# Optimization experiments

Hardware: AMD Instinct MI355X
Metric: run time of the kernel (lower is better)

## Reference

```python
import jax, jax.numpy as jnp
import numpy as np

N, E = 50000, 800000
IN_DIM, HID, HEADS, NUM_CLASSES, NUM_GRAPHS, NUM_LAYERS = 64, 64, 4, 10000, 256, 3
OUT_W = HID * HEADS  # 256


def _gat_layer(x, src, dst, W, a_src, a_dst, b, n_nodes):
    # x: [N, in], W: [heads*out, in], a_src/a_dst: [heads, out], b: [heads*out]
    h = (x @ W.T).reshape(n_nodes, HEADS, HID)            # [N, H, D]
    s_src = jnp.einsum('nhd,hd->nh', h, a_src)            # [N, H]
    s_dst = jnp.einsum('nhd,hd->nh', h, a_dst)
    alpha = jax.nn.leaky_relu(s_src[src] + s_dst[dst], 0.2)  # [E, H]
    m = jax.ops.segment_max(alpha, dst, num_segments=n_nodes)
    m = jnp.where(jnp.isfinite(m), m, 0.0)                # isolated-node safety
    ex = jnp.exp(alpha - m[dst])
    denom = jax.ops.segment_sum(ex, dst, num_segments=n_nodes)
    w = ex / (denom[dst] + 1e-16)                         # PyG softmax epsilon
    out = jax.ops.segment_sum(h[src] * w[:, :, None], dst, num_segments=n_nodes)
    return out.reshape(n_nodes, HEADS * HID) + b


def setup_inputs() -> dict:
    key = jax.random.key(0)
    ks = jax.random.split(key, 20)
    inp = {
        'x': jax.random.normal(ks[0], (N, IN_DIM), jnp.float32),
        'edge_index': jax.random.randint(ks[1], (2, E), 0, N, jnp.int32),
        'batch': jnp.sort(jax.random.randint(ks[2], (N,), 0, NUM_GRAPHS, jnp.int32)),
        'class_label': jax.random.randint(ks[3], (NUM_GRAPHS,), 0, NUM_CLASSES, jnp.int32),
        'emb': jax.random.normal(ks[4], (NUM_CLASSES, HID), jnp.float32),
    }
    in_dims = [IN_DIM + HID, OUT_W, OUT_W]
    for l in range(NUM_LAYERS):
        kw = jax.random.split(ks[5 + l], 4)
        d_in = in_dims[l]
        sc = 1.0 / np.sqrt(d_in)
        inp[f'W{l}'] = jax.random.uniform(kw[0], (OUT_W, d_in), jnp.float32, -sc, sc)
        inp[f'asrc{l}'] = jax.random.uniform(kw[1], (HEADS, HID), jnp.float32, -sc, sc)
        inp[f'adst{l}'] = jax.random.uniform(kw[2], (HEADS, HID), jnp.float32, -sc, sc)
        inp[f'b{l}'] = jnp.zeros((OUT_W,), jnp.float32)
    sc = 1.0 / np.sqrt(OUT_W)
    inp['cls_W'] = jax.random.uniform(ks[10], (1, OUT_W), jnp.float32, -sc, sc)
    inp['cls_b'] = jnp.zeros((1,), jnp.float32)
    return inp


def reference(x, edge_index, batch, class_label, emb,
              W0, asrc0, adst0, b0,
              W1, asrc1, adst1, b1,
              W2, asrc2, adst2, b2,
              cls_W, cls_b):
    n = x.shape[0]
    # template embedding aligned per node
    t = emb[class_label][batch]                          # [N, HID]
    h = jnp.concatenate([x, t], axis=-1)                 # [N, IN+HID]
    # PyG GATConv adds self-loops by default
    loop = jnp.arange(n, dtype=edge_index.dtype)
    src = jnp.concatenate([edge_index[0], loop])
    dst = jnp.concatenate([edge_index[1], loop])
    params = [(W0, asrc0, adst0, b0), (W1, asrc1, adst1, b1), (W2, asrc2, adst2, b2)]
    for (W, a_s, a_d, b) in params:
        h = _gat_layer(h, src, dst, W, a_s, a_d, b, n)
        h = jax.nn.leaky_relu(h, 0.01)                   # F.leaky_relu default slope
    return h @ cls_W.T + cls_b                           # [N, 1]
```

## Files before the change

### kernel.cpp

```cpp
#include <hip/hip_runtime.h>
#include <hip/hip_bf16.h>
#include <hip/hip_fp16.h>
#include <math.h>

#define NNODES 50000
#define NEDGES 800000
#define NBLK 196

typedef __attribute__((ext_vector_type(8))) _Float16 f16x8;
typedef __attribute__((ext_vector_type(4))) _Float16 f16x4;
typedef __attribute__((ext_vector_type(4))) float f32x4;

static __device__ __forceinline__ void gl_lds16(const void* g, void* l) {
    __builtin_amdgcn_global_load_lds(
        (const __attribute__((address_space(1))) void*)g,
        (__attribute__((address_space(3))) void*)l, 16, 0, 0);
}

__global__ void zero_int_kernel(int* __restrict__ p, int n) {
    int i = blockIdx.x * blockDim.x + threadIdx.x;
    if (i < n) p[i] = 0;
}

__global__ void bucket_kernel(const int* __restrict__ ei,
                              int* __restrict__ deg,
                              int* __restrict__ slots) {
    int e = blockIdx.x * blockDim.x + threadIdx.x;
    if (e >= NEDGES) return;
    int d = ei[NEDGES + e];
    int p = atomicAdd(&deg[d], 1);
    if (p < 64) slots[(size_t)d * 64 + p] = ei[e];
}

__global__ void prep_kernel(const float* __restrict__ x,
                            const int* __restrict__ batch,
                            const int* __restrict__ class_label,
                            const float* __restrict__ emb,
                            const float* __restrict__ W0,
                            const float* __restrict__ W1,
                            const float* __restrict__ W2,
                            _Float16* __restrict__ h0,
                            _Float16* __restrict__ F0,
                            _Float16* __restrict__ F1,
                            _Float16* __restrict__ F2) {
    int idx = blockIdx.x * blockDim.x + threadIdx.x;
    const int NH0 = NNODES * 128;
    if (idx < NH0) {
        int n = idx >> 7, c = idx & 127;
        float v;
        if (c < 64) v = x[(n << 6) + c];
        else        v = emb[class_label[batch[n]] * 64 + (c - 64)];
        h0[idx] = (_Float16)v;
    } else {
        int i = idx - NH0;
        if (i < 32768)        F0[i] = (_Float16)W0[i];
        else if (i < 98304)   F1[i - 32768] = (_Float16)W1[i - 32768];
        else if (i < 163840)  F2[i - 98304] = (_Float16)W2[i - 98304];
    }
}

template <int K>
__global__ __launch_bounds__(256) void gemm_mfma_kernel(
        const _Float16* __restrict__ A, const _Float16* __restrict__ W,
        const float* __restrict__ a_src, const float* __restrict__ a_dst,
        _Float16* __restrict__ Cf,
        float* __restrict__ ssrc, float* __restrict__ sdst) {
    __shared__ _Float16 sA[128 * 64];
    __shared__ _Float16 sB[128 * 64];
    const int M = NNODES;
    int tid = threadIdx.x;
    int lane = tid & 63, wave = tid >> 6;
    int wm = wave >> 1, wn = wave & 1;
    int l16 = lane & 15, quad = lane >> 4;
    int bm = blockIdx.x * 128, bn = blockIdx.y * 128;

    int rsub = lane >> 3;
    int kcs = (lane & 7) ^ rsub;
    int sw = l16 & 7;

    f32x4 acc[4][4];
#pragma unroll
    for (int r = 0; r < 4; ++r)
#pragma unroll
        for (int c = 0; c < 4; ++c) acc[r][c] = (f32x4){0.f, 0.f, 0.f, 0.f};

    const int NST = K / 64;
#pragma unroll
    for (int s = 0; s < NST; ++s) {
        int ks = s * 64;
        __syncthreads();
#pragma unroll
        for (int j = 0; j < 4; ++j) {
            int seg = wave * 4 + j;
            int r = seg * 8 + rsub;
            int acol = ks + kcs * 8;
            int garow = bm + r; if (garow > M - 1) garow = M - 1;
            gl_lds16(A + (size_t)garow * K + acol, &sA[seg * 512]);
            gl_lds16(W + (size_t)(bn + r) * K + acol, &sB[seg * 512]);
        }
        __syncthreads();
#pragma unroll
        for (int ks32 = 0; ks32 < 2; ++ks32) {
            f16x8 af[4], bf[4];
#pragma unroll
            for (int r = 0; r < 4; ++r) {
                int row = wm * 64 + r * 16 + l16;
                af[r] = *(const f16x8*)&sA[row * 64 + ((ks32 * 4 + quad) ^ sw) * 8];
            }
#pragma unroll
            for (int c = 0; c < 4; ++c) {
                int row = wn * 64 + c * 16 + l16;
                bf[c] = *(const f16x8*)&sB[row * 64 + ((ks32 * 4 + quad) ^ sw) * 8];
            }
#pragma unroll
            for (int r = 0; r < 4; ++r)
#pragma unroll
                for (int c = 0; c < 4; ++c)
                    acc[r][c] = __builtin_amdgcn_mfma_f32_16x16x32_f16(
                        af[r], bf[c], acc[r][c], 0, 0, 0);
        }
    }

    int headblk = (bn + wn * 64) >> 6;
    float asv[4], adv[4];
#pragma unroll
    for (int c = 0; c < 4; ++c) {
        asv[c] = a_src[headblk * 64 + c * 16 + l16];
        adv[c] = a_dst[headblk * 64 + c * 16 + l16];
    }
#pragma unroll
    for (int r = 0; r < 4; ++r) {
        int gr0 = bm + wm * 64 + r * 16 + quad * 4;
        f32x4 ps = {0.f, 0.f, 0.f, 0.f}, pd = {0.f, 0.f, 0.f, 0.f};
#pragma unroll
        for (int c = 0; c < 4; ++c) {
            int gc = bn + wn * 64 + c * 16 + l16;
#pragma unroll
            for (int reg = 0; reg < 4; ++reg) {
                float v = acc[r][c][reg];
                ps[reg] += v * asv[c];
                pd[reg] += v * adv[c];
                int grow = gr0 + reg;
                if (grow < M) Cf[(size_t)grow * 256 + gc] = (_Float16)v;
            }
        }
#pragma unroll
        for (int off = 1; off < 16; off <<= 1) {
#pragma unroll
            for (int reg = 0; reg < 4; ++reg) {
                ps[reg] += __shfl_xor(ps[reg], off, 64);
                pd[reg] += __shfl_xor(pd[reg], off, 64);
            }
        }
        if (l16 == 0) {
#pragma unroll
            for (int reg = 0; reg < 4; ++reg) {
                int grow = gr0 + reg;
                if (grow < M) {
                    ssrc[grow * 4 + headblk] = ps[reg];
                    sdst[grow * 4 + headblk] = pd[reg];
                }
            }
        }
    }
}

__device__ __forceinline__ float sel4(float4 v, int head) {
    float r = v.x;
    r = (head == 1) ? v.y : r;
    r = (head == 2) ? v.z : r;
    r = (head == 3) ? v.w : r;
    return r;
}

template <bool LAST>
__global__ __launch_bounds__(256) void aggregate_kernel(
        const _Float16* __restrict__ hpf,
        const float* __restrict__ ssrc,
        const float* __restrict__ sdst,
        const int* __restrict__ deg,
        const int* __restrict__ slots,
        const float* __restrict__ bias,
        _Float16* __restrict__ out_h,
        const float* __restrict__ cls_W,
        const float* __restrict__ cls_b,
        float* __restrict__ out) {
    __shared__ __align__(16) float s_w[4][64][4];
    __shared__ int s_idx[4][64];
    int lane = threadIdx.x & 63;
    int slot = threadIdx.x >> 6;
    int n = blockIdx.x * 4 + slot;
    if (n >= NNODES) return;
    int head = lane >> 4;
    int dn = deg[n]; if (dn > 64) dn = 64;
    float4 sd = ((const float4*)sdst)[n];
    const f16x4* hp4 = (const f16x4*)hpf;

    float4 ssl = ((const float4*)ssrc)[n];
    float ax = ssl.x + sd.x, ay = ssl.y + sd.y;
    float az = ssl.z + sd.z, aw = ssl.w + sd.w;
    ax = ax > 0.f ? ax : 0.2f * ax;
    ay = ay > 0.f ? ay : 0.2f * ay;
    az = az > 0.f ? az : 0.2f * az;
    aw = aw > 0.f ? aw : 0.2f * aw;
    float4 exs = {__expf(ax), __expf(ay), __expf(az), __expf(aw)};
    float wself = sel4(exs, head);
    f16x4 vs = hp4[(size_t)n * 64 + lane];
    float dsum = wself;
    float4 acc = {wself * (float)vs.x, wself * (float)vs.y,
                  wself * (float)vs.z, wself * (float)vs.w};

    float4 ex = {0.f, 0.f, 0.f, 0.f};
    int s = 0;
    if (lane < dn) {
        s = slots[(size_t)n * 64 + lane];
        float4 ss = ((const float4*)ssrc)[s];
        float bx = ss.x + sd.x, by = ss.y + sd.y;
        float bz = ss.z + sd.z, bw = ss.w + sd.w;
        bx = bx > 0.f ? bx : 0.2f * bx;
        by = by > 0.f ? by : 0.2f * by;
        bz = bz > 0.f ? bz : 0.2f * bz;
        bw = bw > 0.f ? bw : 0.2f * bw;
        ex.x = __expf(bx); ex.y = __expf(by);
        ex.z = __expf(bz); ex.w = __expf(bw);
    }
    *(float4*)&s_w[slot][lane][0] = ex;
    s_idx[slot][lane] = s;

    int e = 0;
    for (; e + 8 <= dn; e += 8) {
        int si[8]; float w[8]; f16x4 v[8];
#pragma unroll
        for (int t = 0; t < 8; ++t) {
            si[t] = s_idx[slot][e + t];
            w[t] = s_w[slot][e + t][head];
        }
#pragma unroll
        for (int t = 0; t < 8; ++t) v[t] = hp4[(size_t)si[t] * 64 + lane];
#pragma unroll
        for (int t = 0; t < 8; ++t) {
            dsum += w[t];
            acc.x += w[t] * (float)v[t].x;
            acc.y += w[t] * (float)v[t].y;
            acc.z += w[t] * (float)v[t].z;
            acc.w += w[t] * (float)v[t].w;
        }
    }
    for (; e < dn; ++e) {
        int si = s_idx[slot][e];
        float w = s_w[slot][e][head];
        f16x4 v = hp4[(size_t)si * 64 + lane];
        dsum += w;
        acc.x += w * (float)v.x; acc.y += w * (float)v.y;
        acc.z += w * (float)v.z; acc.w += w * (float)v.w;
    }

    float inv = 1.f / (dsum + 1e-16f);
    float4 bv = ((const float4*)bias)[lane];
    float4 o;
    o.x = acc.x * inv + bv.x;
    o.y = acc.y * inv + bv.y;
    o.z = acc.z * inv + bv.z;
    o.w = acc.w * inv + bv.w;
    o.x = o.x > 0.f ? o.x : 0.01f * o.x;
    o.y = o.y > 0.f ? o.y : 0.01f * o.y;
    o.z = o.z > 0.f ? o.z : 0.01f * o.z;
    o.w = o.w > 0.f ? o.w : 0.01f * o.w;

    if (!LAST) {
        f16x4 ov = {(_Float16)o.x, (_Float16)o.y, (_Float16)o.z, (_Float16)o.w};
        ((f16x4*)out_h)[(size_t)n * 64 + lane] = ov;
    } else {
        float4 wv = ((const float4*)cls_W)[lane];
        float sdot = o.x * wv.x + o.y * wv.y + o.z * wv.z + o.w * wv.w;
#pragma unroll
        for (int off = 1; off < 64; off <<= 1)
            sdot += __shfl_xor(sdot, off, 64);
        if (lane == 0) out[n] = sdot + cls_b[0];
    }
}

extern "C" void kernel_launch(void* const* d_in, const int* in_sizes, int n_in,
                              void* d_out, int out_size, void* d_ws, size_t ws_size,
                              hipStream_t stream) {
    const float* x     = (const float*)d_in[0];
    const int*   ei    = (const int*)d_in[1];
    const int*   batch = (const int*)d_in[2];
    const int*   clab  = (const int*)d_in[3];
    const float* emb   = (const float*)d_in[4];
    const float* W[3]    = {(const float*)d_in[5], (const float*)d_in[9],  (const float*)d_in[13]};
    const float* asrc[3] = {(const float*)d_in[6], (const float*)d_in[10], (const float*)d_in[14]};
    const float* adst[3] = {(const float*)d_in[7], (const float*)d_in[11], (const float*)d_in[15]};
    const float* bias[3] = {(const float*)d_in[8], (const float*)d_in[12], (const float*)d_in[16]};
    const float* clsW = (const float*)d_in[17];
    const float* clsb = (const float*)d_in[18];
    float* out = (float*)d_out;

    char* ws = (char*)d_ws;
    size_t off = 0;
    auto alloc = [&](size_t bytes) {
        void* p = ws + off;
        off += (bytes + 255) & ~(size_t)255;
        return p;
    };
    _Float16* Cf   = (_Float16*)alloc((size_t)NNODES * 256 * 2);
    _Float16* hA   = (_Float16*)alloc((size_t)NNODES * 256 * 2);
    _Float16* h0f  = (_Float16*)alloc((size_t)NNODES * 128 * 2);
    _Float16* Wf[3];
    Wf[0] = (_Float16*)alloc((size_t)256 * 128 * 2);
    Wf[1] = (_Float16*)alloc((size_t)256 * 256 * 2);
    Wf[2] = (_Float16*)alloc((size_t)256 * 256 * 2);
    float* ssrc  = (float*)alloc((size_t)NNODES * 4 * 4);
    float* sdst  = (float*)alloc((size_t)NNODES * 4 * 4);
    int*   deg   = (int*)alloc((size_t)NNODES * 4);
    int*   slots = (int*)alloc((size_t)NNODES * 64 * 4);
    (void)ws_size; (void)in_sizes; (void)n_in; (void)out_size;

    zero_int_kernel<<<dim3(NBLK), dim3(256), 0, stream>>>(deg, NNODES);
    bucket_kernel<<<dim3((NEDGES + 255) / 256), dim3(256), 0, stream>>>(ei, deg, slots);

    const int NPREP = NNODES * 128 + 163840;
    prep_kernel<<<dim3((NPREP + 255) / 256), dim3(256), 0, stream>>>(
        x, batch, clab, emb, W[0], W[1], W[2], h0f, Wf[0], Wf[1], Wf[2]);

    dim3 gemm_grid((NNODES + 127) / 128, 2);
    dim3 node_grid((NNODES + 3) / 4);
    for (int l = 0; l < 3; ++l) {
        if (l == 0)
            gemm_mfma_kernel<128><<<gemm_grid, 256, 0, stream>>>(
                h0f, Wf[0], asrc[0], adst[0], Cf, ssrc, sdst);
        else
            gemm_mfma_kernel<256><<<gemm_grid, 256, 0, stream>>>(
                hA, Wf[l], asrc[l], adst[l], Cf, ssrc, sdst);
        if (l < 2)
            aggregate_kernel<false><<<node_grid, 256, 0, stream>>>(
                Cf, ssrc, sdst, deg, slots, bias[l],
                hA, nullptr, nullptr, nullptr);
        else
            aggregate_kernel<true><<<node_grid, 256, 0, stream>>>(
                Cf, ssrc, sdst, deg, slots, bias[l],
                nullptr, clsW, clsb, out);
    }
}
```

Before: 410.8 us.

## Fuse all GNN stages into one persistent cooperative kernel with grid syncs

Replaces the chain of separate launches with one cooperative persistent kernel. Inside it, prep, GEMM and aggregation run as grid-stride loops separated by grid.sync. The deg zeroing is folded into prep, and the edge bucketing runs on a quarter of the blocks while the other blocks do the layer-0 GEMM, so the two overlap. This removes launch gaps and adds concurrency, at the cost of grid-wide barriers and occupancy capped by the persistent grid (4 blocks/CU, 32KB shared), which may reduce latency hiding in the gather-heavy aggregation. Separate kernels remain as a fallback if the cooperative launch fails.

```diff
diff --git a/kernel.cpp b/kernel.cpp
--- a/kernel.cpp
+++ b/kernel.cpp
@@ -1,15 +1,33 @@
 #include <hip/hip_runtime.h>
-#include <hip/hip_bf16.h>
 #include <hip/hip_fp16.h>
+#include <hip/hip_cooperative_groups.h>
 #include <math.h>
+
+namespace cg = cooperative_groups;
 
 #define NNODES 50000
 #define NEDGES 800000
-#define NBLK 196
+#define NT_TILES (((NNODES + 127) / 128) * 2)
+#define NGROUPS ((NNODES + 3) / 4)
+#define NH0 (NNODES * 128)
+#define NPREP (NH0 + 163840 + NNODES)
 
 typedef __attribute__((ext_vector_type(8))) _Float16 f16x8;
 typedef __attribute__((ext_vector_type(4))) _Float16 f16x4;
 typedef __attribute__((ext_vector_type(4))) float f32x4;
+
+struct GnnParams {
+    const float* x; const int* ei; const int* batch; const int* clab;
+    const float* emb;
+    const float* W0; const float* W1; const float* W2;
+    const float* as0; const float* ad0; const float* b0;
+    const float* as1; const float* ad1; const float* b1;
+    const float* as2; const float* ad2; const float* b2;
+    const float* clsW; const float* clsb; float* out;
+    _Float16* Cf; _Float16* hA; _Float16* h0f;
+    _Float16* Wf0; _Float16* Wf1; _Float16* Wf2;
+    float* ssrc; float* sdst; int* deg; int* slots;
+};
 
 static __device__ __forceinline__ void gl_lds16(const void* g, void* l) {
     __builtin_amdgcn_global_load_lds(
@@ -17,328 +35,372 @@
         (__attribute__((address_space(3))) void*)l, 16, 0, 0);
 }
 
-__global__ void zero_int_kernel(int* __restrict__ p, int n) {
-    int i = blockIdx.x * blockDim.x + threadIdx.x;
-    if (i < n) p[i] = 0;
-}
-
-__global__ void bucket_kernel(const int* __restrict__ ei,
-                              int* __restrict__ deg,
-                              int* __restrict__ slots) {
-    int e = blockIdx.x * blockDim.x + threadIdx.x;
-    if (e >= NEDGES) return;
-    int d = ei[NEDGES + e];
-    int p = atomicAdd(&deg[d], 1);
-    if (p < 64) slots[(size_t)d * 64 + p] = ei[e];
-}
-
-__global__ void prep_kernel(const float* __restrict__ x,
-                            const int* __restrict__ batch,
-                            const int* __restrict__ class_label,
-                            const float* __restrict__ emb,
-                            const float* __restrict__ W0,
-                            const float* __restrict__ W1,
-                            const float* __restrict__ W2,
-                            _Float16* __restrict__ h0,
-                            _Float16* __restrict__ F0,
-                            _Float16* __restrict__ F1,
-                            _Float16* __restrict__ F2) {
-    int idx = blockIdx.x * blockDim.x + threadIdx.x;
-    const int NH0 = NNODES * 128;
-    if (idx < NH0) {
-        int n = idx >> 7, c = idx & 127;
-        float v;
-        if (c < 64) v = x[(n << 6) + c];
-        else        v = emb[class_label[batch[n]] * 64 + (c - 64)];
-        h0[idx] = (_Float16)v;
-    } else {
-        int i = idx - NH0;
-        if (i < 32768)        F0[i] = (_Float16)W0[i];
-        else if (i < 98304)   F1[i - 32768] = (_Float16)W1[i - 32768];
-        else if (i < 163840)  F2[i - 98304] = (_Float16)W2[i - 98304];
+static __device__ __forceinline__ float sel4(float4 v, int head) {
+    float r = v.x;
+    r = (head == 1) ? v.y : r;
+    r = (head == 2) ? v.z : r;
+    r = (head == 3) ? v.w : r;
+    return r;
+}
+
+static __device__ void prep_dev(const GnnParams& p, int b0, int nblk) {
+    for (int idx = b0 * 256 + (int)threadIdx.x; idx < NPREP; idx += nblk * 256) {
+        if (idx < NH0) {
+            int n = idx >> 7, c = idx & 127;
+            float v;
+            if (c < 64) v = p.x[(n << 6) + c];
+            else        v = p.emb[p.clab[p.batch[n]] * 64 + (c - 64)];
+            p.h0f[idx] = (_Float16)v;
+        } else {
+            int i = idx - NH0;
+            if (i < 32768)        p.Wf0[i] = (_Float16)p.W0[i];
+            else if (i < 98304)   p.Wf1[i - 32768] = (_Float16)p.W1[i - 32768];
+            else if (i < 163840)  p.Wf2[i - 98304] = (_Float16)p.W2[i - 98304];
+            else                  p.deg[i - 163840] = 0;
+        }
     }
 }
 
+static __device__ void bucket_dev(const int* __restrict__ ei,
+                                  int* __restrict__ deg,
+                                  int* __restrict__ slots,
+                                  int relblk, int nblk) {
+    for (int e = relblk * 256 + (int)threadIdx.x; e < NEDGES; e += nblk * 256) {
+        int d = ei[NEDGES + e];
+        int pos = atomicAdd(&deg[d], 1);
+        if (pos < 64) slots[(size_t)d * 64 + pos] = ei[e];
+    }
+}
+
 template <int K>
-__global__ __launch_bounds__(256) void gemm_mfma_kernel(
-        const _Float16* __restrict__ A, const _Float16* __restrict__ W,
-        const float* __restrict__ a_src, const float* __restrict__ a_dst,
-        _Float16* __restrict__ Cf,
-        float* __restrict__ ssrc, float* __restrict__ sdst) {
-    __shared__ _Float16 sA[128 * 64];
-    __shared__ _Float16 sB[128 * 64];
+static __device__ void gemm_dev(const _Float16* __restrict__ A,
+                                const _Float16* __restrict__ Wt,
+                                const float* __restrict__ a_src,
+                                const float* __restrict__ a_dst,
+                                _Float16* __restrict__ Cf,
+                                float* __restrict__ ssrc, float* __restrict__ sdst,
+                                char* smem, int t0, int tstride) {
+    _Float16* sA = (_Float16*)smem;
+    _Float16* sB = (_Float16*)(smem + 16384);
     const int M = NNODES;
     int tid = threadIdx.x;
     int lane = tid & 63, wave = tid >> 6;
     int wm = wave >> 1, wn = wave & 1;
     int l16 = lane & 15, quad = lane >> 4;
-    int bm = blockIdx.x * 128, bn = blockIdx.y * 128;
-
     int rsub = lane >> 3;
     int kcs = (lane & 7) ^ rsub;
     int sw = l16 & 7;
 
-    f32x4 acc[4][4];
-#pragma unroll
-    for (int r = 0; r < 4; ++r)
-#pragma unroll
-        for (int c = 0; c < 4; ++c) acc[r][c] = (f32x4){0.f, 0.f, 0.f, 0.f};
-
-    const int NST = K / 64;
-#pragma unroll
-    for (int s = 0; s < NST; ++s) {
-        int ks = s * 64;
-        __syncthreads();
-#pragma unroll
-        for (int j = 0; j < 4; ++j) {
-            int seg = wave * 4 + j;
-            int r = seg * 8 + rsub;
-            int acol = ks + kcs * 8;
-            int garow = bm + r; if (garow > M - 1) garow = M - 1;
-            gl_lds16(A + (size_t)garow * K + acol, &sA[seg * 512]);
-            gl_lds16(W + (size_t)(bn + r) * K + acol, &sB[seg * 512]);
-        }
-        __syncthreads();
-#pragma unroll
-        for (int ks32 = 0; ks32 < 2; ++ks32) {
-            f16x8 af[4], bf[4];
-#pragma unroll
-            for (int r = 0; r < 4; ++r) {
-                int row = wm * 64 + r * 16 + l16;
-                af[r] = *(const f16x8*)&sA[row * 64 + ((ks32 * 4 + quad) ^ sw) * 8];
-            }
+    for (int tile = t0; tile < NT_TILES; tile += tstride) {
+        int bm = (tile >> 1) * 128, bn = (tile & 1) * 128;
+        f32x4 acc[4][4];
+#pragma unroll
+        for (int r = 0; r < 4; ++r)
+#pragma unroll
+            for (int c = 0; c < 4; ++c) acc[r][c] = (f32x4){0.f, 0.f, 0.f, 0.f};
+
+#pragma unroll
+        for (int s = 0; s < K / 64; ++s) {
+            int ks = s * 64;
+            __syncthreads();
+#pragma unroll
+            for (int j = 0; j < 4; ++j) {
+                int seg = wave * 4 + j;
+                int r = seg * 8 + rsub;
+                int acol = ks + kcs * 8;
+                int garow = bm + r; if (garow > M - 1) garow = M - 1;
+                gl_lds16(A + (size_t)garow * K + acol, &sA[seg * 512]);
+                gl_lds16(Wt + (size_t)(bn + r) * K + acol, &sB[seg * 512]);
+            }
+            __syncthreads();
+#pragma unroll
+            for (int ks32 = 0; ks32 < 2; ++ks32) {
+                f16x8 af[4], bf[4];
+#pragma unroll
+                for (int r = 0; r < 4; ++r) {
+                    int row = wm * 64 + r * 16 + l16;
+                    af[r] = *(const f16x8*)&sA[row * 64 + ((ks32 * 4 + quad) ^ sw) * 8];
+                }
+#pragma unroll
+                for (int c = 0; c < 4; ++c) {
+                    int row = wn * 64 + c * 16 + l16;
+                    bf[c] = *(const f16x8*)&sB[row * 64 + ((ks32 * 4 + quad) ^ sw) * 8];
+                }
+#pragma unroll
+                for (int r = 0; r < 4; ++r)
+#pragma unroll
+                    for (int c = 0; c < 4; ++c)
+                        acc[r][c] = __builtin_amdgcn_mfma_f32_16x16x32_f16(
+                            af[r], bf[c], acc[r][c], 0, 0, 0);
+            }
+        }
+
+        int headblk = (bn + wn * 64) >> 6;
+        float asv[4], adv[4];
+#pragma unroll
+        for (int c = 0; c < 4; ++c) {
+            asv[c] = a_src[headblk * 64 + c * 16 + l16];
+            adv[c] = a_dst[headblk * 64 + c * 16 + l16];
+        }
+#pragma unroll
+        for (int r = 0; r < 4; ++r) {
+            int gr0 = bm + wm * 64 + r * 16 + quad * 4;
+            f32x4 ps = {0.f, 0.f, 0.f, 0.f}, pd = {0.f, 0.f, 0.f, 0.f};
 #pragma unroll
             for (int c = 0; c < 4; ++c) {
-                int row = wn * 64 + c * 16 + l16;
-                bf[c] = *(const f16x8*)&sB[row * 64 + ((ks32 * 4 + quad) ^ sw) * 8];
-            }
-#pragma unroll
-            for (int r = 0; r < 4; ++r)
-#pragma unroll
-                for (int c = 0; c < 4; ++c)
-                    acc[r][c] = __builtin_amdgcn_mfma_f32_16x16x32_f16(
-                        af[r], bf[c], acc[r][c], 0, 0, 0);
+                int gc = bn + wn * 64 + c * 16 + l16;
+#pragma unroll
+                for (int reg = 0; reg < 4; ++reg) {
+                    float v = acc[r][c][reg];
+                    ps[reg] += v * asv[c];
+                    pd[reg] += v * adv[c];
+                    int grow = gr0 + reg;
+                    if (grow < M) Cf[(size_t)grow * 256 + gc] = (_Float16)v;
+                }
+            }
+#pragma unroll
+            for (int off = 1; off < 16; off <<= 1) {
+#pragma unroll
+                for (int reg = 0; reg < 4; ++reg) {
+                    ps[reg] += __shfl_xor(ps[reg], off, 64);
+                    pd[reg] += __shfl_xor(pd[reg], off, 64);
+                }
+            }
+            if (l16 == 0) {
+#pragma unroll
+                for (int reg = 0; reg < 4; ++reg) {
+                    int grow = gr0 + reg;
+                    if (grow < M) {
+                        ssrc[grow * 4 + headblk] = ps[reg];
+                        sdst[grow * 4 + headblk] = pd[reg];
+                    }
+                }
+            }
         }
     }
-
-    int headblk = (bn + wn * 64) >> 6;
-    float asv[4], adv[4];
-#pragma unroll
-    for (int c = 0; c < 4; ++c) {
-        asv[c] = a_src[headblk * 64 + c * 16 + l16];
-        adv[c] = a_dst[headblk * 64 + c * 16 + l16];
+}
+
+static __device__ void agg_dev(const _Float16* __restrict__ hpf,
+                               const float* __restrict__ ssrc,
+                               const float* __restrict__ sdst,
+                               const int* __restrict__ deg,
+                               const int* __restrict__ slots,
+                               const float* __restrict__ bias,
+                               _Float16* __restrict__ out_h,
+                               const float* __restrict__ cls_W,
+                               const float* __restrict__ cls_b,
+                               float* __restrict__ out,
+                               bool last, char* smem, int g0, int gstride) {
+    float (*s_w)[64][4] = (float (*)[64][4])smem;
+    int (*s_idx)[64] = (int (*)[64])(smem + 4096);
+    int lane = threadIdx.x & 63;
+    int wslot = threadIdx.x >> 6;
+    int head = lane >> 4;
+    const f16x4* hp4 = (const f16x4*)hpf;
+
+    for (int g = g0; g < NGROUPS; g += gstride) {
+        int n = g * 4 + wslot;
+        if (n >= NNODES) continue;
+        int dn = deg[n]; if (dn > 64) dn = 64;
+        float4 sd = ((const float4*)sdst)[n];
+
+        float4 ssl = ((const float4*)ssrc)[n];
+        float ax = ssl.x + sd.x, ay = ssl.y + sd.y;
+        float az = ssl.z + sd.z, aw = ssl.w + sd.w;
+        ax = ax > 0.f ? ax : 0.2f * ax;
+        ay = ay > 0.f ? ay : 0.2f * ay;
+        az = az > 0.f ? az : 0.2f * az;
+        aw = aw > 0.f ? aw : 0.2f * aw;
+        float4 exs = {__expf(ax), __expf(ay), __expf(az), __expf(aw)};
+        float wself = sel4(exs, head);
+        f16x4 vs = hp4[(size_t)n * 64 + lane];
+        float dsum = wself;
+        float4 acc = {wself * (float)vs.x, wself * (float)vs.y,
+                      wself * (float)vs.z, wself * (float)vs.w};
+
+        float4 ex = {0.f, 0.f, 0.f, 0.f};
+        int s = 0;
+        if (lane < dn) {
+            s = slots[(size_t)n * 64 + lane];
+            float4 ss = ((const float4*)ssrc)[s];
+            float bx = ss.x + sd.x, by = ss.y + sd.y;
+            float bz = ss.z + sd.z, bw = ss.w + sd.w;
+            bx = bx > 0.f ? bx : 0.2f * bx;
+            by = by > 0.f ? by : 0.2f * by;
+            bz = bz > 0.f ? bz : 0.2f * bz;
+            bw = bw > 0.f ? bw : 0.2f * bw;
+            ex.x = __expf(bx); ex.y = __expf(by);
+            ex.z = __expf(bz); ex.w = __expf(bw);
+        }
+        *(float4*)&s_w[wslot][lane][0] = ex;
+        s_idx[wslot][lane] = s;
+
+        int e = 0;
+        for (; e + 8 <= dn; e += 8) {
+            int si[8]; float w[8]; f16x4 v[8];
+#pragma unroll
+            for (int t = 0; t < 8; ++t) {
+                si[t] = s_idx[wslot][e + t];
+                w[t] = s_w[wslot][e + t][head];
+            }
+#pragma unroll
+            for (int t = 0; t < 8; ++t) v[t] = hp4[(size_t)si[t] * 64 + lane];
+#pragma unroll
+            for (int t = 0; t < 8; ++t) {
+                dsum += w[t];
+                acc.x += w[t] * (float)v[t].x;
+                acc.y += w[t] * (float)v[t].y;
+                acc.z += w[t] * (float)v[t].z;
+                acc.w += w[t] * (float)v[t].w;
+            }
+        }
+        for (; e < dn; ++e) {
+            int si = s_idx[wslot][e];
+            float w = s_w[wslot][e][head];
+            f16x4 v = hp4[(size_t)si * 64 + lane];
+            dsum += w;
+            acc.x += w * (float)v.x; acc.y += w * (float)v.y;
+            acc.z += w * (float)v.z; acc.w += w * (float)v.w;
+        }
+
+        float inv = 1.f / (dsum + 1e-16f);
+        float4 bv = ((const float4*)bias)[lane];
+        float4 o;
+        o.x = acc.x * inv + bv.x;
+        o.y = acc.y * inv + bv.y;
+        o.z = acc.z * inv + bv.z;
+        o.w = acc.w * inv + bv.w;
+        o.x = o.x > 0.f ? o.x : 0.01f * o.x;
+        o.y = o.y > 0.f ? o.y : 0.01f * o.y;
+        o.z = o.z > 0.f ? o.z : 0.01f * o.z;
+        o.w = o.w > 0.f ? o.w : 0.01f * o.w;
+
+        if (!last) {
+            f16x4 ov = {(_Float16)o.x, (_Float16)o.y, (_Float16)o.z, (_Float16)o.w};
+            ((f16x4*)out_h)[(size_t)n * 64 + lane] = ov;
+        } else {
+            float4 wv = ((const float4*)cls_W)[lane];
+            float sdot = o.x * wv.x + o.y * wv.y + o.z * wv.z + o.w * wv.w;
+#pragma unroll
+            for (int off = 1; off < 64; off <<= 1)
+                sdot += __shfl_xor(sdot, off, 64);
+            if (lane == 0) out[n] = sdot + cls_b[0];
+        }
     }
-#pragma unroll
-    for (int r = 0; r < 4; ++r) {
-        int gr0 = bm + wm * 64 + r * 16 + quad * 4;
-        f32x4 ps = {0.f, 0.f, 0.f, 0.f}, pd = {0.f, 0.f, 0.f, 0.f};
-#pragma unroll
-        for (int c = 0; c < 4; ++c) {
-            int gc = bn + wn * 64 + c * 16 + l16;
-#pragma unroll
-            for (int reg = 0; reg < 4; ++reg) {
-                float v = acc[r][c][reg];
-                ps[reg] += v * asv[c];
-                pd[reg] += v * adv[c];
-                int grow = gr0 + reg;
-                if (grow < M) Cf[(size_t)grow * 256 + gc] = (_Float16)v;
-            }
-        }
-#pragma unroll
-        for (int off = 1; off < 16; off <<= 1) {
-#pragma unroll
-            for (int reg = 0; reg < 4; ++reg) {
-                ps[reg] += __shfl_xor(ps[reg], off, 64);
-                pd[reg] += __shfl_xor(pd[reg], off, 64);
-            }
-        }
-        if (l16 == 0) {
-#pragma unroll
-            for (int reg = 0; reg < 4; ++reg) {
-                int grow = gr0 + reg;
-                if (grow < M) {
-                    ssrc[grow * 4 + headblk] = ps[reg];
-                    sdst[grow * 4 + headblk] = pd[reg];
-                }
-            }
-        }
-    }
-}
-
-__device__ __forceinline__ float sel4(float4 v, int head) {
-    float r = v.x;
-    r = (head == 1) ? v.y : r;
-    r = (head == 2) ? v.z : r;
-    r = (head == 3) ? v.w : r;
-    return r;
+}
+
+__global__ __launch_bounds__(256, 4) void fused_gnn(GnnParams p, int nb) {
+    __shared__ __align__(16) char smem[32768];
+    cg::grid_group grid = cg::this_grid();
+
+    prep_dev(p, blockIdx.x, nb);
+    __threadfence(); grid.sync();
+
+    int G0 = (nb * 3) >> 2; if (G0 < 1) G0 = 1; if (G0 >= nb) G0 = nb - 1;
+    if ((int)blockIdx.x < G0)
+        gemm_dev<128>(p.h0f, p.Wf0, p.as0, p.ad0, p.Cf, p.ssrc, p.sdst,
+                      smem, blockIdx.x, G0);
+    else
+        bucket_dev(p.ei, p.deg, p.slots, blockIdx.x - G0, nb - G0);
+    __threadfence(); grid.sync();
+
+    agg_dev(p.Cf, p.ssrc, p.sdst, p.deg, p.slots, p.b0, p.hA,
+            nullptr, nullptr, nullptr, false, smem, blockIdx.x, nb);
+    __threadfence(); grid.sync();
+
+    gemm_dev<256>(p.hA, p.Wf1, p.as1, p.ad1, p.Cf, p.ssrc, p.sdst,
+                  smem, blockIdx.x, nb);
+    __threadfence(); grid.sync();
+
+    agg_dev(p.Cf, p.ssrc, p.sdst, p.deg, p.slots, p.b1, p.hA,
+            nullptr, nullptr, nullptr, false, smem, blockIdx.x, nb);
+    __threadfence(); grid.sync();
+
+    gemm_dev<256>(p.hA, p.Wf2, p.as2, p.ad2, p.Cf, p.ssrc, p.sdst,
+                  smem, blockIdx.x, nb);
+    __threadfence(); grid.sync();
+
+    agg_dev(p.Cf, p.ssrc, p.sdst, p.deg, p.slots, p.b2, nullptr,
+            p.clsW, p.clsb, p.out, true, smem, blockIdx.x, nb);
+}
+
+__global__ void prep_kernel(GnnParams p) { prep_dev(p, blockIdx.x, gridDim.x); }
+
+__global__ void bucket_kernel(GnnParams p) {
+    bucket_dev(p.ei, p.deg, p.slots, blockIdx.x, gridDim.x);
+}
+
+template <int K>
+__global__ __launch_bounds__(256) void gemm_kernel(GnnParams p,
+        const _Float16* A, const _Float16* Wt,
+        const float* as, const float* ad) {
+    __shared__ __align__(16) char smem[32768];
+    gemm_dev<K>(A, Wt, as, ad, p.Cf, p.ssrc, p.sdst, smem, blockIdx.x, gridDim.x);
 }
 
 template <bool LAST>
-__global__ __launch_bounds__(256) void aggregate_kernel(
-        const _Float16* __restrict__ hpf,
-        const float* __restrict__ ssrc,
-        const float* __restrict__ sdst,
-        const int* __restrict__ deg,
-        const int* __restrict__ slots,
-        const float* __restrict__ bias,
-        _Float16* __restrict__ out_h,
-        const float* __restrict__ cls_W,
-        const float* __restrict__ cls_b,
-        float* __restrict__ out) {
-    __shared__ __align__(16) float s_w[4][64][4];
-    __shared__ int s_idx[4][64];
-    int lane = threadIdx.x & 63;
-    int slot = threadIdx.x >> 6;
-    int n = blockIdx.x * 4 + slot;
-    if (n >= NNODES) return;
-    int head = lane >> 4;
-    int dn = deg[n]; if (dn > 64) dn = 64;
-    float4 sd = ((const float4*)sdst)[n];
-    const f16x4* hp4 = (const f16x4*)hpf;
-
-    float4 ssl = ((const float4*)ssrc)[n];
-    float ax = ssl.x + sd.x, ay = ssl.y + sd.y;
-    float az = ssl.z + sd.z, aw = ssl.w + sd.w;
-    ax = ax > 0.f ? ax : 0.2f * ax;
-    ay = ay > 0.f ? ay : 0.2f * ay;
-    az = az > 0.f ? az : 0.2f * az;
-    aw = aw > 0.f ? aw : 0.2f * aw;
-    float4 exs = {__expf(ax), __expf(ay), __expf(az), __expf(aw)};
-    float wself = sel4(exs, head);
-    f16x4 vs = hp4[(size_t)n * 64 + lane];
-    float dsum = wself;
-    float4 acc = {wself * (float)vs.x, wself * (float)vs.y,
-                  wself * (float)vs.z, wself * (float)vs.w};
-
-    float4 ex = {0.f, 0.f, 0.f, 0.f};
-    int s = 0;
-    if (lane < dn) {
-        s = slots[(size_t)n * 64 + lane];
-        float4 ss = ((const float4*)ssrc)[s];
-        float bx = ss.x + sd.x, by = ss.y + sd.y;
-        float bz = ss.z + sd.z, bw = ss.w + sd.w;
-        bx = bx > 0.f ? bx : 0.2f * bx;
-        by = by > 0.f ? by : 0.2f * by;
-        bz = bz > 0.f ? bz : 0.2f * bz;
-        bw = bw > 0.f ? bw : 0.2f * bw;
-        ex.x = __expf(bx); ex.y = __expf(by);
-        ex.z = __expf(bz); ex.w = __expf(bw);
-    }
-    *(float4*)&s_w[slot][lane][0] = ex;
-    s_idx[slot][lane] = s;
-
-    int e = 0;
-    for (; e + 8 <= dn; e += 8) {
-        int si[8]; float w[8]; f16x4 v[8];
-#pragma unroll
-        for (int t = 0; t < 8; ++t) {
-            si[t] = s_idx[slot][e + t];
-            w[t] = s_w[slot][e + t][head];
-        }
-#pragma unroll
-        for (int t = 0; t < 8; ++t) v[t] = hp4[(size_t)si[t] * 64 + lane];
-#pragma unroll
-        for (int t = 0; t < 8; ++t) {
-            dsum += w[t];
-            acc.x += w[t] * (float)v[t].x;
-            acc.y += w[t] * (float)v[t].y;
-            acc.z += w[t] * (float)v[t].z;
-            acc.w += w[t] * (float)v[t].w;
-        }
-    }
-    for (; e < dn; ++e) {
-        int si = s_idx[slot][e];
-        float w = s_w[slot][e][head];
-        f16x4 v = hp4[(size_t)si * 64 + lane];
-        dsum += w;
-        acc.x += w * (float)v.x; acc.y += w * (float)v.y;
-        acc.z += w * (float)v.z; acc.w += w * (float)v.w;
-    }
-
-    float inv = 1.f / (dsum + 1e-16f);
-    float4 bv = ((const float4*)bias)[lane];
-    float4 o;
-    o.x = acc.x * inv + bv.x;
-    o.y = acc.y * inv + bv.y;
-    o.z = acc.z * inv + bv.z;
-    o.w = acc.w * inv + bv.w;
-    o.x = o.x > 0.f ? o.x : 0.01f * o.x;
-    o.y = o.y > 0.f ? o.y : 0.01f * o.y;
-    o.z = o.z > 0.f ? o.z : 0.01f * o.z;
-    o.w = o.w > 0.f ? o.w : 0.01f * o.w;
-
-    if (!LAST) {
-        f16x4 ov = {(_Float16)o.x, (_Float16)o.y, (_Float16)o.z, (_Float16)o.w};
-        ((f16x4*)out_h)[(size_t)n * 64 + lane] = ov;
-    } else {
-        float4 wv = ((const float4*)cls_W)[lane];
-        float sdot = o.x * wv.x + o.y * wv.y + o.z * wv.z + o.w * wv.w;
-#pragma unroll
-        for (int off = 1; off < 64; off <<= 1)
-            sdot += __shfl_xor(sdot, off, 64);
-        if (lane == 0) out[n] = sdot + cls_b[0];
-    }
+__global__ __launch_bounds__(256) void agg_kernel(GnnParams p, const float* bias) {
+    __shared__ __align__(16) char smem[5120];
+    agg_dev(p.Cf, p.ssrc, p.sdst, p.deg, p.slots, bias,
+            p.hA, p.clsW, p.clsb, p.out, LAST, smem, blockIdx.x, gridDim.x);
 }
 
 extern "C" void kernel_launch(void* const* d_in, const int* in_sizes, int n_in,
                               void* d_out, int out_size, void* d_ws, size_t ws_size,
                               hipStream_t stream) {
-    const float* x     = (const float*)d_in[0];
-    const int*   ei    = (const int*)d_in[1];
-    const int*   batch = (const int*)d_in[2];
-    const int*   clab  = (const int*)d_in[3];
-    const float* emb   = (const float*)d_in[4];
-    const float* W[3]    = {(const float*)d_in[5], (const float*)d_in[9],  (const float*)d_in[13]};
-    const float* asrc[3] = {(const float*)d_in[6], (const float*)d_in[10], (const float*)d_in[14]};
-    const float* adst[3] = {(const float*)d_in[7], (const float*)d_in[11], (const float*)d_in[15]};
-    const float* bias[3] = {(const float*)d_in[8], (const float*)d_in[12], (const float*)d_in[16]};
-    const float* clsW = (const float*)d_in[17];
-    const float* clsb = (const float*)d_in[18];
-    float* out = (float*)d_out;
+    GnnParams p;
+    p.x     = (const float*)d_in[0];
+    p.ei    = (const int*)d_in[1];
+    p.batch = (const int*)d_in[2];
+    p.clab  = (const int*)d_in[3];
+    p.emb   = (const float*)d_in[4];
+    p.W0 = (const float*)d_in[5];  p.as0 = (const float*)d_in[6];
+    p.ad0 = (const float*)d_in[7]; p.b0 = (const float*)d_in[8];
+    p.W1 = (const float*)d_in[9];  p.as1 = (const float*)d_in[10];
+    p.ad1 = (const float*)d_in[11]; p.b1 = (const float*)d_in[12];
+    p.W2 = (const float*)d_in[13]; p.as2 = (const float*)d_in[14];
+    p.ad2 = (const float*)d_in[15]; p.b2 = (const float*)d_in[16];
+    p.clsW = (const float*)d_in[17];
+    p.clsb = (const float*)d_in[18];
+    p.out  = (float*)d_out;
 
     char* ws = (char*)d_ws;
     size_t off = 0;
     auto alloc = [&](size_t bytes) {
-        void* p = ws + off;
+        void* q = ws + off;
         off += (bytes + 255) & ~(size_t)255;
-        return p;
+        return q;
     };
-    _Float16* Cf   = (_Float16*)alloc((size_t)NNODES * 256 * 2);
-    _Float16* hA   = (_Float16*)alloc((size_t)NNODES * 256 * 2);
-    _Float16* h0f  = (_Float16*)alloc((size_t)NNODES * 128 * 2);
-    _Float16* Wf[3];
-    Wf[0] = (_Float16*)alloc((size_t)256 * 128 * 2);
-    Wf[1] = (_Float16*)alloc((size_t)256 * 256 * 2);
-    Wf[2] = (_Float16*)alloc((size_t)256 * 256 * 2);
-    float* ssrc  = (float*)alloc((size_t)NNODES * 4 * 4);
-    float* sdst  = (float*)alloc((size_t)NNODES * 4 * 4);
-    int*   deg   = (int*)alloc((size_t)NNODES * 4);
-    int*   slots = (int*)alloc((size_t)NNODES * 64 * 4);
+    p.Cf   = (_Float16*)alloc((size_t)NNODES * 256 * 2);
+    p.hA   = (_Float16*)alloc((size_t)NNODES * 256 * 2);
+    p.h0f  = (_Float16*)alloc((size_t)NNODES * 128 * 2);
+    p.Wf0  = (_Float16*)alloc((size_t)256 * 128 * 2);
+    p.Wf1  = (_Float16*)alloc((size_t)256 * 256 * 2);
+    p.Wf2  = (_Float16*)alloc((size_t)256 * 256 * 2);
+    p.ssrc = (float*)alloc((size_t)NNODES * 4 * 4);
+    p.sdst = (float*)alloc((size_t)NNODES * 4 * 4);
+    p.deg  = (int*)alloc((size_t)NNODES * 4);
+    p.slots = (int*)alloc((size_t)NNODES * 64 * 4);
     (void)ws_size; (void)in_sizes; (void)n_in; (void)out_size;
 
-    zero_int_kernel<<<dim3(NBLK), dim3(256), 0, stream>>>(deg, NNODES);
-    bucket_kernel<<<dim3((NEDGES + 255) / 256), dim3(256), 0, stream>>>(ei, deg, slots);
-
-    const int NPREP = NNODES * 128 + 163840;
-    prep_kernel<<<dim3((NPREP + 255) / 256), dim3(256), 0, stream>>>(
-        x, batch, clab, emb, W[0], W[1], W[2], h0f, Wf[0], Wf[1], Wf[2]);
-
-    dim3 gemm_grid((NNODES + 127) / 128, 2);
-    dim3 node_grid((NNODES + 3) / 4);
-    for (int l = 0; l < 3; ++l) {
-        if (l == 0)
-            gemm_mfma_kernel<128><<<gemm_grid, 256, 0, stream>>>(
-                h0f, Wf[0], asrc[0], adst[0], Cf, ssrc, sdst);
-        else
-            gemm_mfma_kernel<256><<<gemm_grid, 256, 0, stream>>>(
-                hA, Wf[l], asrc[l], adst[l], Cf, ssrc, sdst);
-        if (l < 2)
-            aggregate_kernel<false><<<node_grid, 256, 0, stream>>>(
-                Cf, ssrc, sdst, deg, slots, bias[l],
-                hA, nullptr, nullptr, nullptr);
-        else
-            aggregate_kernel<true><<<node_grid, 256, 0, stream>>>(
-                Cf, ssrc, sdst, deg, slots, bias[l],
-                nullptr, clsW, clsb, out);
+    int occ = 0;
+    hipError_t oe = hipOccupancyMaxActiveBlocksPerMultiprocessor(&occ, fused_gnn, 256, 0);
+    bool launched = false;
+    if (oe == hipSuccess && occ > 0) {
+        int nb = occ * 256;
+        if (nb > NGROUPS) nb = NGROUPS;
+        void* args[] = { (void*)&p, (void*)&nb };
+        launched = (hipLaunchCooperativeKernel(fused_gnn, dim3(nb), dim3(256),
+                                               args, 0, stream) == hipSuccess);
     }
-}
+    if (launched) return;
+
+    prep_kernel<<<dim3((NPREP + 255) / 256), dim3(256), 0, stream>>>(p);
+    bucket_kernel<<<dim3((NEDGES + 255) / 256), dim3(256), 0, stream>>>(p);
+    gemm_kernel<128><<<dim3(NT_TILES), dim3(256), 0, stream>>>(p, p.h0f, p.Wf0, p.as0, p.ad0);
+    agg_kernel<false><<<dim3(NGROUPS), dim3(256), 0, stream>>>(p, p.b0);
+    gemm_kernel<256><<<dim3(NT_TILES), dim3(256), 0, stream>>>(p, p.hA, p.Wf1, p.as1, p.ad1);
+    agg_kernel<false><<<dim3(NGROUPS), dim3(256), 0, stream>>>(p, p.b1);
+    gemm_kernel<256><<<dim3(NT_TILES), dim3(256), 0, stream>>>(p, p.hA, p.Wf2, p.as2, p.ad2);
+    agg_kernel<true><<<dim3(NGROUPS), dim3(256), 0, stream>>>(p, p.b2);
+}
```

After: 459.2 us. +11.8%, slower.

## Fuse edge bucketing into layer-0 GEMM kernel and replace zero kernel with memset

Applied to the files above, without the earlier changes.

The layer-0 GEMM and the edge-bucketing pass now run in one launch. Even-numbered blocks compute GEMM tiles and odd-numbered blocks run a grid-stride loop that bucket-inserts edges, so the memory-bound atomic work can overlap with the MFMA compute. The separate degree-zeroing kernel is replaced by hipMemsetAsync. This removes two launches and their serialization, but the interleaved blocks contend for CU resources, and the bucket blocks reserve unused 32KB of LDS.

```diff
diff --git a/kernel.cpp b/kernel.cpp
--- a/kernel.cpp
+++ b/kernel.cpp
@@ -1,11 +1,13 @@
 #include <hip/hip_runtime.h>
-#include <hip/hip_bf16.h>
 #include <hip/hip_fp16.h>
 #include <math.h>
 
 #define NNODES 50000
 #define NEDGES 800000
-#define NBLK 196
+#define NT_TILES (((NNODES + 127) / 128) * 2)
+#define NGROUPS ((NNODES + 3) / 4)
+#define NH0 (NNODES * 128)
+#define NPREP (NH0 + 163840)
 
 typedef __attribute__((ext_vector_type(8))) _Float16 f16x8;
 typedef __attribute__((ext_vector_type(4))) _Float16 f16x4;
@@ -17,19 +19,12 @@
         (__attribute__((address_space(3))) void*)l, 16, 0, 0);
 }
 
-__global__ void zero_int_kernel(int* __restrict__ p, int n) {
-    int i = blockIdx.x * blockDim.x + threadIdx.x;
-    if (i < n) p[i] = 0;
-}
-
-__global__ void bucket_kernel(const int* __restrict__ ei,
-                              int* __restrict__ deg,
-                              int* __restrict__ slots) {
-    int e = blockIdx.x * blockDim.x + threadIdx.x;
-    if (e >= NEDGES) return;
-    int d = ei[NEDGES + e];
-    int p = atomicAdd(&deg[d], 1);
-    if (p < 64) slots[(size_t)d * 64 + p] = ei[e];
+static __device__ __forceinline__ float sel4(float4 v, int head) {
+    float r = v.x;
+    r = (head == 1) ? v.y : r;
+    r = (head == 2) ? v.z : r;
+    r = (head == 3) ? v.w : r;
+    return r;
 }
 
 __global__ void prep_kernel(const float* __restrict__ x,
@@ -44,7 +39,6 @@
                             _Float16* __restrict__ F1,
                             _Float16* __restrict__ F2) {
     int idx = blockIdx.x * blockDim.x + threadIdx.x;
-    const int NH0 = NNODES * 128;
     if (idx < NH0) {
         int n = idx >> 7, c = idx & 127;
         float v;
@@ -60,20 +54,21 @@
 }
 
 template <int K>
-__global__ __launch_bounds__(256) void gemm_mfma_kernel(
-        const _Float16* __restrict__ A, const _Float16* __restrict__ W,
-        const float* __restrict__ a_src, const float* __restrict__ a_dst,
-        _Float16* __restrict__ Cf,
-        float* __restrict__ ssrc, float* __restrict__ sdst) {
-    __shared__ _Float16 sA[128 * 64];
-    __shared__ _Float16 sB[128 * 64];
+static __device__ void gemm_tile_dev(const _Float16* __restrict__ A,
+                                     const _Float16* __restrict__ W,
+                                     const float* __restrict__ a_src,
+                                     const float* __restrict__ a_dst,
+                                     _Float16* __restrict__ Cf,
+                                     float* __restrict__ ssrc,
+                                     float* __restrict__ sdst,
+                                     char* smem, int bm, int bn) {
+    _Float16* sA = (_Float16*)smem;
+    _Float16* sB = (_Float16*)(smem + 16384);
     const int M = NNODES;
     int tid = threadIdx.x;
     int lane = tid & 63, wave = tid >> 6;
     int wm = wave >> 1, wn = wave & 1;
     int l16 = lane & 15, quad = lane >> 4;
-    int bm = blockIdx.x * 128, bn = blockIdx.y * 128;
-
     int rsub = lane >> 3;
     int kcs = (lane & 7) ^ rsub;
     int sw = l16 & 7;
@@ -84,9 +79,8 @@
 #pragma unroll
         for (int c = 0; c < 4; ++c) acc[r][c] = (f32x4){0.f, 0.f, 0.f, 0.f};
 
-    const int NST = K / 64;
-#pragma unroll
-    for (int s = 0; s < NST; ++s) {
+#pragma unroll
+    for (int s = 0; s < K / 64; ++s) {
         int ks = s * 64;
         __syncthreads();
 #pragma unroll
@@ -165,12 +159,40 @@
     }
 }
 
-__device__ __forceinline__ float sel4(float4 v, int head) {
-    float r = v.x;
-    r = (head == 1) ? v.y : r;
-    r = (head == 2) ? v.z : r;
-    r = (head == 3) ? v.w : r;
-    return r;
+template <int K>
+__global__ __launch_bounds__(256) void gemm_mfma_kernel(
+        const _Float16* __restrict__ A, const _Float16* __restrict__ W,
+        const float* __restrict__ a_src, const float* __restrict__ a_dst,
+        _Float16* __restrict__ Cf,
+        float* __restrict__ ssrc, float* __restrict__ sdst) {
+    __shared__ __align__(16) char smem[32768];
+    gemm_tile_dev<K>(A, W, a_src, a_dst, Cf, ssrc, sdst, smem,
+                     blockIdx.x * 128, blockIdx.y * 128);
+}
+
+__global__ __launch_bounds__(256) void gemm0_bucket_kernel(
+        const _Float16* __restrict__ A, const _Float16* __restrict__ W,
+        const float* __restrict__ a_src, const float* __restrict__ a_dst,
+        _Float16* __restrict__ Cf,
+        float* __restrict__ ssrc, float* __restrict__ sdst,
+        const int* __restrict__ ei,
+        int* __restrict__ deg, int* __restrict__ slots) {
+    __shared__ __align__(16) char smem[32768];
+    int b = blockIdx.x;
+    if ((b & 1) == 0) {
+        int tile = b >> 1;
+        if (tile < NT_TILES)
+            gemm_tile_dev<128>(A, W, a_src, a_dst, Cf, ssrc, sdst, smem,
+                               (tile >> 1) * 128, (tile & 1) * 128);
+    } else {
+        int rel = b >> 1;
+        int stride = NT_TILES * 256;
+        for (int e = rel * 256 + (int)threadIdx.x; e < NEDGES; e += stride) {
+            int d = ei[NEDGES + e];
+            int pos = atomicAdd(&deg[d], 1);
+            if (pos < 64) slots[(size_t)d * 64 + pos] = ei[e];
+        }
+    }
 }
 
 template <bool LAST>
@@ -316,29 +338,26 @@
     int*   slots = (int*)alloc((size_t)NNODES * 64 * 4);
     (void)ws_size; (void)in_sizes; (void)n_in; (void)out_size;
 
-    zero_int_kernel<<<dim3(NBLK), dim3(256), 0, stream>>>(deg, NNODES);
-    bucket_kernel<<<dim3((NEDGES + 255) / 256), dim3(256), 0, stream>>>(ei, deg, slots);
-
-    const int NPREP = NNODES * 128 + 163840;
+    hipMemsetAsync(deg, 0, (size_t)NNODES * 4, stream);
+
     prep_kernel<<<dim3((NPREP + 255) / 256), dim3(256), 0, stream>>>(
         x, batch, clab, emb, W[0], W[1], W[2], h0f, Wf[0], Wf[1], Wf[2]);
 
     dim3 gemm_grid((NNODES + 127) / 128, 2);
-    dim3 node_grid((NNODES + 3) / 4);
-    for (int l = 0; l < 3; ++l) {
-        if (l == 0)
-            gemm_mfma_kernel<128><<<gemm_grid, 256, 0, stream>>>(
-                h0f, Wf[0], asrc[0], adst[0], Cf, ssrc, sdst);
-        else
-            gemm_mfma_kernel<256><<<gemm_grid, 256, 0, stream>>>(
-                hA, Wf[l], asrc[l], adst[l], Cf, ssrc, sdst);
-        if (l < 2)
-            aggregate_kernel<false><<<node_grid, 256, 0, stream>>>(
-                Cf, ssrc, sdst, deg, slots, bias[l],
-                hA, nullptr, nullptr, nullptr);
-        else
-            aggregate_kernel<true><<<node_grid, 256, 0, stream>>>(
-                Cf, ssrc, sdst, deg, slots, bias[l],
-                nullptr, clsW, clsb, out);
-    }
-}
+    dim3 node_grid(NGROUPS);
+
+    gemm0_bucket_kernel<<<dim3(NT_TILES * 2), dim3(256), 0, stream>>>(
+        h0f, Wf[0], asrc[0], adst[0], Cf, ssrc, sdst, ei, deg, slots);
+    aggregate_kernel<false><<<node_grid, dim3(256), 0, stream>>>(
+        Cf, ssrc, sdst, deg, slots, bias[0], hA, nullptr, nullptr, nullptr);
+
+    gemm_mfma_kernel<256><<<gemm_grid, dim3(256), 0, stream>>>(
+        hA, Wf[1], asrc[1], adst[1], Cf, ssrc, sdst);
+    aggregate_kernel<false><<<node_grid, dim3(256), 0, stream>>>(
+        Cf, ssrc, sdst, deg, slots, bias[1], hA, nullptr, nullptr, nullptr);
+
+    gemm_mfma_kernel<256><<<gemm_grid, dim3(256), 0, stream>>>(
+        hA, Wf[2], asrc[2], adst[2], Cf, ssrc, sdst);
+    aggregate_kernel<true><<<node_grid, dim3(256), 0, stream>>>(
+        Cf, ssrc, sdst, deg, slots, bias[2], nullptr, clsW, clsb, out);
+}
```

Result: faster. 383.4 us (-6.7%).
